# Kernel optimization log

Measured on AMD Instinct MI355X. Metric: run time of the kernel, lower is better.

The kernel has to match this reference:

```python
import jax, jax.numpy as jnp
import numpy as np

N = 50000      # nodes
E = 800000     # edges (avg degree 16)
IN_DIM = 128
HID = 64       # num_hidden
HEADS = 1
NUM_LAYERS = 3       # -> 4 SNATConv layers total
SLOPE = 0.2          # negative_slope
THR = 0.01           # threhold: edges with attention < THR are pruned after layer 0


def setup_inputs() -> dict:
    key = jax.random.key(0)
    ks = jax.random.split(key, 16)
    s = 0.05
    x = jax.random.normal(ks[0], (N, IN_DIM), jnp.float32)
    edge_src = jax.random.randint(ks[1], (E,), 0, N)
    edge_dst = jax.random.randint(ks[2], (E,), 0, N)
    W_embed = jax.random.normal(ks[3], (IN_DIM, HID), jnp.float32) * s
    n_conv = NUM_LAYERS + 1
    # all conv layers map HID*HEADS -> HEADS*HID (heads==1 so square)
    W_gat = jax.random.normal(ks[4], (n_conv, HID, HEADS * HID), jnp.float32) * s
    a_l = jax.random.normal(ks[5], (n_conv, HEADS, HID), jnp.float32) * s
    a_r = jax.random.normal(ks[6], (n_conv, HEADS, HID), jnp.float32) * s
    d_cat = (NUM_LAYERS + 1) * HID
    W0 = jax.random.normal(ks[7], (d_cat, HID), jnp.float32) * s
    b0 = jnp.zeros((HID,), jnp.float32)
    W1 = jax.random.normal(ks[8], (HID, HID), jnp.float32) * s
    b1 = jnp.zeros((HID,), jnp.float32)
    W2 = jax.random.normal(ks[9], (HID, 1), jnp.float32) * s
    b2 = jnp.zeros((1,), jnp.float32)
    return {"x": x, "edge_src": edge_src, "edge_dst": edge_dst,
            "W_embed": W_embed, "W_gat": W_gat, "a_l": a_l, "a_r": a_r,
            "W0": W0, "b0": b0, "W1": W1, "b1": b1, "W2": W2, "b2": b2}


def _edge_softmax(e, dst):
    # e: [E, H] raw scores; softmax over incoming edges of each dst node
    m = jax.ops.segment_max(e, dst, num_segments=N)       # [N, H]
    a = jnp.exp(e - m[dst])
    s = jax.ops.segment_sum(a, dst, num_segments=N)       # [N, H]
    return a / jnp.maximum(s[dst], 1e-9)


def _snat_conv(h, W, al, ar, src, dst, mask):
    # h: [N, F_in]; W: [F_in, H*HID]; al/ar: [H, HID]
    feat = (h @ W).reshape(N, HEADS, HID)                 # [N, H, HID]
    el = jnp.sum(feat * al, axis=-1)                      # [N, H]
    er = jnp.sum(feat * ar, axis=-1)
    e = jax.nn.leaky_relu(el[src] + er[dst], SLOPE)       # [E, H]
    if mask is not None:
        e = jnp.where(mask, e, -1e9)                      # prune thresholded edges
    alpha = _edge_softmax(e, dst)                         # [E, H]
    out = jax.ops.segment_sum(feat[src] * alpha[..., None], dst, num_segments=N)
    return jax.nn.elu(out), alpha                         # [N, H, HID], [E, H]


def reference(x, edge_src, edge_dst, W_embed, W_gat, a_l, a_r, W0, b0, W1, b1, W2, b2):
    src, dst = edge_src, edge_dst
    h = jnp.tanh(x @ W_embed)                             # [N, HID]
    # layer 0: computes attention and the threshold mask (index_1 / index_0)
    h0, alpha = _snat_conv(h, W_gat[0], a_l[0], a_r[0], src, dst, None)
    mask = alpha >= THR                                   # [E, H] kept-edge mask
    h = h0.reshape(N, HEADS * HID)
    H_cat = [h]
    for l in range(1, NUM_LAYERS):                        # middle layers reuse mask
        hl, _ = _snat_conv(h, W_gat[l], a_l[l], a_r[l], src, dst, mask)
        h = hl.reshape(N, HEADS * HID)
        H_cat.append(h)
    feats, _ = _snat_conv(h, W_gat[NUM_LAYERS], a_l[NUM_LAYERS], a_r[NUM_LAYERS], src, dst, mask)
    feats = feats.mean(axis=1)                            # [N, HID] mean over heads
    f = jnp.concatenate(H_cat + [feats], axis=1)          # [N, (L+1)*HID]
    out = jax.nn.relu(f @ W0 + b0)                        # activationP
    out = jax.nn.relu(out @ W1 + b1)
    out = jax.nn.relu(out @ W2 + b2)                      # final F.relu
    return out                                            # [N, 1]
```

## Files before the change

kernel.cpp:

```cpp
#include <hip/hip_runtime.h>
#include <math.h>


__global__ void k_zero(int* __restrict__ counts, int N) {
  int i = blockIdx.x * 256 + threadIdx.x;
  if (i < N) counts[i] = 0;
}

__global__ void k_hist(const int* __restrict__ dst, int* __restrict__ counts, int E) {
  int e = blockIdx.x * blockDim.x + threadIdx.x;
  if (e < E) atomicAdd(&counts[dst[e]], 1);
}

__global__ __launch_bounds__(1024) void k_bsum(const int* __restrict__ counts,
                                               int* __restrict__ bsum, int n) {
  __shared__ int wsum[16];
  int tid = threadIdx.x, lane = tid & 63, wid = tid >> 6;
  int i = blockIdx.x * 1024 + tid;
  int v = (i < n) ? counts[i] : 0;
  #pragma unroll
  for (int off = 32; off; off >>= 1) v += __shfl_xor(v, off, 64);
  if (lane == 0) wsum[wid] = v;
  __syncthreads();
  if (wid == 0) {
    int w = (lane < 16) ? wsum[lane] : 0;
    #pragma unroll
    for (int off = 8; off; off >>= 1) w += __shfl_xor(w, off, 64);
    if (lane == 0) bsum[blockIdx.x] = w;
  }
}

__global__ __launch_bounds__(64) void k_bscan(const int* __restrict__ bsum,
                                              int* __restrict__ bofs,
                                              int* __restrict__ row_ptr,
                                              int nb, int n) {
  int lane = threadIdx.x;
  int carry = 0;
  for (int base = 0; base < nb; base += 64) {
    int idx = base + lane;
    int orig = (idx < nb) ? bsum[idx] : 0;
    int inc = orig;
    #pragma unroll
    for (int off = 1; off < 64; off <<= 1) {
      int t = __shfl_up(inc, off, 64);
      if (lane >= off) inc += t;
    }
    if (idx < nb) bofs[idx] = carry + inc - orig;
    carry += __shfl(inc, 63, 64);
  }
  if (lane == 0) row_ptr[n] = carry;
}

__global__ __launch_bounds__(1024) void k_scan3(const int* __restrict__ counts,
                                                const int* __restrict__ bofs,
                                                int* __restrict__ row_ptr,
                                                int* __restrict__ cursor, int n) {
  __shared__ int wsum[16];
  int tid = threadIdx.x, lane = tid & 63, wid = tid >> 6;
  int i = blockIdx.x * 1024 + tid;
  int v = (i < n) ? counts[i] : 0;
  int inc = v;
  #pragma unroll
  for (int off = 1; off < 64; off <<= 1) {
    int t = __shfl_up(inc, off, 64);
    if (lane >= off) inc += t;
  }
  if (lane == 63) wsum[wid] = inc;
  __syncthreads();
  if (wid == 0 && lane < 16) {
    int orig = wsum[lane];
    int w = orig;
    #pragma unroll
    for (int off = 1; off < 16; off <<= 1) {
      int t = __shfl_up(w, off, 64);
      if (lane >= off) w += t;
    }
    wsum[lane] = w - orig;
  }
  __syncthreads();
  int excl = bofs[blockIdx.x] + wsum[wid] + inc - v;
  if (i < n) { row_ptr[i] = excl; cursor[i] = excl; }
}

__global__ void k_scatter(const int* __restrict__ src, const int* __restrict__ dst,
                          int* __restrict__ cursor, int* __restrict__ csr_src, int E) {
  int e = blockIdx.x * blockDim.x + threadIdx.x;
  if (e < E) {
    int pos = atomicAdd(&cursor[dst[e]], 1);
    csr_src[pos] = src[e];
  }
}

__global__ __launch_bounds__(256, 4) void k_embed_feat(
    const float* __restrict__ x, const float* __restrict__ We,
    const float* __restrict__ Wg, const float* __restrict__ al,
    const float* __restrict__ ar, float* __restrict__ feat,
    float* __restrict__ el, float* __restrict__ er, int N) {
  __shared__ float sA[64 * 129];
  __shared__ float sE[64 * 8];
  int tid = threadIdx.x, lane = tid & 63, wv = tid >> 6;
  int nb0 = blockIdx.x * 64, nl = N - 1;
  int r = tid >> 2, p = tid & 3;
  {
    const float* gp = x + (size_t)min(nb0 + r, nl) * 128;
    #pragma unroll
    for (int half = 0; half < 2; half++) {
      const float* g = gp + half * 64 + p * 16;
      float4 v0 = *(const float4*)(g + 0), v1 = *(const float4*)(g + 4);
      float4 v2 = *(const float4*)(g + 8), v3 = *(const float4*)(g + 12);
      float* dp = &sA[r * 129 + half * 64 + p * 16];
      dp[0]=v0.x; dp[1]=v0.y; dp[2]=v0.z; dp[3]=v0.w;
      dp[4]=v1.x; dp[5]=v1.y; dp[6]=v1.z; dp[7]=v1.w;
      dp[8]=v2.x; dp[9]=v2.y; dp[10]=v2.z; dp[11]=v2.w;
      dp[12]=v3.x; dp[13]=v3.y; dp[14]=v3.z; dp[15]=v3.w;
    }
  }
  __syncthreads();
  int f0 = __builtin_amdgcn_readfirstlane(wv * 16);
  float acc[16];
  #pragma unroll
  for (int f = 0; f < 16; f++) acc[f] = 0.f;
  #pragma unroll 8
  for (int k = 0; k < 128; k++) {
    float ak = sA[lane * 129 + k];
    const float* wr = We + k * 64 + f0;
    #pragma unroll
    for (int f = 0; f < 16; f++) acc[f] = fmaf(ak, wr[f], acc[f]);
  }
  __syncthreads();
  #pragma unroll
  for (int f = 0; f < 16; f++) sA[lane * 65 + f0 + f] = tanhf(acc[f]);
  __syncthreads();
  float acc2[16];
  #pragma unroll
  for (int f = 0; f < 16; f++) acc2[f] = 0.f;
  #pragma unroll 8
  for (int k = 0; k < 64; k++) {
    float ak = sA[lane * 65 + k];
    const float* wr = Wg + k * 64 + f0;
    #pragma unroll
    for (int f = 0; f < 16; f++) acc2[f] = fmaf(ak, wr[f], acc2[f]);
  }
  float rl = 0.f, rr = 0.f;
  #pragma unroll
  for (int f = 0; f < 16; f++) {
    rl = fmaf(acc2[f], al[f0 + f], rl);
    rr = fmaf(acc2[f], ar[f0 + f], rr);
  }
  sE[lane * 8 + wv] = rl;
  sE[lane * 8 + 4 + wv] = rr;
  __syncthreads();
  #pragma unroll
  for (int f = 0; f < 16; f++) sA[lane * 65 + f0 + f] = acc2[f];
  __syncthreads();
  {
    int n = nb0 + r;
    if (n < N) {
      const float* sp = &sA[r * 65 + p * 16];
      float* gp = feat + (size_t)n * 64 + p * 16;
      #pragma unroll
      for (int q = 0; q < 4; q++)
        *(float4*)(gp + q * 4) = make_float4(sp[q*4+0], sp[q*4+1], sp[q*4+2], sp[q*4+3]);
    }
  }
  if (tid < 64) {
    int n = nb0 + tid;
    if (n < N) {
      el[n] = (sE[tid*8+0] + sE[tid*8+1]) + (sE[tid*8+2] + sE[tid*8+3]);
      er[n] = (sE[tid*8+4] + sE[tid*8+5]) + (sE[tid*8+6] + sE[tid*8+7]);
    }
  }
}

__global__ __launch_bounds__(256, 4) void k_feat(const float* __restrict__ hin,
                                                 const float* __restrict__ Wg,
                                                 const float* __restrict__ al,
                                                 const float* __restrict__ ar,
                                                 float* __restrict__ feat,
                                                 float* __restrict__ el,
                                                 float* __restrict__ er, int N) {
  __shared__ float sA[64 * 65];
  __shared__ float sE[64 * 8];
  int tid = threadIdx.x, lane = tid & 63, wv = tid >> 6;
  int nb0 = blockIdx.x * 64;
  int nl = N - 1;
  int r = tid >> 2, p = tid & 3;
  {
    const float* g = hin + (size_t)min(nb0 + r, nl) * 64 + p * 16;
    float4 v0 = *(const float4*)(g + 0), v1 = *(const float4*)(g + 4);
    float4 v2 = *(const float4*)(g + 8), v3 = *(const float4*)(g + 12);
    float* dp = &sA[r * 65 + p * 16];
    dp[0]=v0.x; dp[1]=v0.y; dp[2]=v0.z; dp[3]=v0.w;
    dp[4]=v1.x; dp[5]=v1.y; dp[6]=v1.z; dp[7]=v1.w;
    dp[8]=v2.x; dp[9]=v2.y; dp[10]=v2.z; dp[11]=v2.w;
    dp[12]=v3.x; dp[13]=v3.y; dp[14]=v3.z; dp[15]=v3.w;
  }
  __syncthreads();
  int f0 = __builtin_amdgcn_readfirstlane(wv * 16);
  float acc[16];
  #pragma unroll
  for (int f = 0; f < 16; f++) acc[f] = 0.f;
  #pragma unroll 8
  for (int k = 0; k < 64; k++) {
    float ak = sA[lane * 65 + k];
    const float* wr = Wg + k * 64 + f0;
    #pragma unroll
    for (int f = 0; f < 16; f++) acc[f] = fmaf(ak, wr[f], acc[f]);
  }
  float rl = 0.f, rr = 0.f;
  #pragma unroll
  for (int f = 0; f < 16; f++) {
    rl = fmaf(acc[f], al[f0 + f], rl);
    rr = fmaf(acc[f], ar[f0 + f], rr);
  }
  __syncthreads();
  #pragma unroll
  for (int f = 0; f < 16; f++) sA[lane * 65 + f0 + f] = acc[f];
  sE[lane * 8 + wv] = rl;
  sE[lane * 8 + 4 + wv] = rr;
  __syncthreads();
  {
    int n = nb0 + r;
    if (n < N) {
      const float* sp = &sA[r * 65 + p * 16];
      float* gp = feat + (size_t)n * 64 + p * 16;
      #pragma unroll
      for (int q = 0; q < 4; q++)
        *(float4*)(gp + q * 4) = make_float4(sp[q*4+0], sp[q*4+1], sp[q*4+2], sp[q*4+3]);
    }
  }
  if (tid < 64) {
    int n = nb0 + tid;
    if (n < N) {
      el[n] = (sE[tid*8+0] + sE[tid*8+1]) + (sE[tid*8+2] + sE[tid*8+3]);
      er[n] = (sE[tid*8+4] + sE[tid*8+5]) + (sE[tid*8+6] + sE[tid*8+7]);
    }
  }
}

__global__ __launch_bounds__(256) void k_aggr(const float* __restrict__ feat,
                                              const float* __restrict__ el,
                                              const float* __restrict__ er,
                                              const int* __restrict__ row_ptr,
                                              const int* __restrict__ csr_src,
                                              unsigned char* __restrict__ mask,
                                              int write_mask, int use_mask,
                                              float* __restrict__ hout, int N) {
  __shared__ __align__(16) int   su[4][64];
  __shared__ __align__(16) float spl[4][64];
  int wv = (int)((blockIdx.x * blockDim.x + threadIdx.x) >> 6);
  int wave = threadIdx.x >> 6, lane = threadIdx.x & 63;
  if (wv >= N) return;
  int beg = row_ptr[wv], end = row_ptr[wv + 1];
  int deg = end - beg;
  float erv = er[wv];
  float acc0 = 0.f, acc1 = 0.f, acc2 = 0.f, acc3 = 0.f;
  if (deg <= 64) {
    int k = beg + lane;
    bool have = (lane < deg);
    int u = have ? csr_src[k] : 0;
    float sc = -INFINITY;
    if (have) {
      float e0 = el[u] + erv;
      sc = (e0 >= 0.f) ? e0 : 0.2f * e0;
      if (use_mask && mask[k] == 0) sc = -1e9f;
    }
    float m = sc;
    #pragma unroll
    for (int off = 32; off; off >>= 1) m = fmaxf(m, __shfl_xor(m, off, 64));
    float pl = have ? expf(sc - m) : 0.f;
    float s = pl;
    #pragma unroll
    for (int off = 32; off; off >>= 1) s += __shfl_xor(s, off, 64);
    pl *= 1.0f / fmaxf(s, 1e-9f);
    if (write_mask && have) mask[k] = (pl >= 0.01f) ? 1 : 0;
    su[wave][lane] = u;
    spl[wave][lane] = pl;
    int dq = (deg + 3) >> 2;
    #pragma unroll 2
    for (int q = 0; q < dq; q++) {
      int4   uu = *(const int4*)&su[wave][q * 4];
      float4 pp = *(const float4*)&spl[wave][q * 4];
      acc0 = fmaf(pp.x, feat[(size_t)uu.x * 64 + lane], acc0);
      acc1 = fmaf(pp.y, feat[(size_t)uu.y * 64 + lane], acc1);
      acc2 = fmaf(pp.z, feat[(size_t)uu.z * 64 + lane], acc2);
      acc3 = fmaf(pp.w, feat[(size_t)uu.w * 64 + lane], acc3);
    }
  } else {
    float m = -INFINITY, s = 0.f;
    for (int base = beg; base < end; base += 64) {
      int k = base + lane;
      float sc = -INFINITY;
      if (k < end) {
        int u = csr_src[k];
        float e0 = el[u] + erv;
        sc = (e0 >= 0.f) ? e0 : 0.2f * e0;
        if (use_mask && mask[k] == 0) sc = -1e9f;
      }
      float cm = sc;
      #pragma unroll
      for (int off = 32; off; off >>= 1) cm = fmaxf(cm, __shfl_xor(cm, off, 64));
      float nm = fmaxf(m, cm);
      float t = (k < end) ? expf(sc - nm) : 0.f;
      #pragma unroll
      for (int off = 32; off; off >>= 1) t += __shfl_xor(t, off, 64);
      s = s * expf(m - nm) + t;
      m = nm;
    }
    float inv = 1.0f / fmaxf(s, 1e-9f);
    for (int base = beg; base < end; base += 64) {
      int k = base + lane;
      int u = 0;
      float pl = 0.f;
      if (k < end) {
        u = csr_src[k];
        float e0 = el[u] + erv;
        float sc = (e0 >= 0.f) ? e0 : 0.2f * e0;
        if (use_mask && mask[k] == 0) sc = -1e9f;
        pl = expf(sc - m) * inv;
        if (write_mask) mask[k] = (pl >= 0.01f) ? 1 : 0;
      }
      su[wave][lane] = u;
      spl[wave][lane] = pl;
      int cnt = min(64, end - base);
      int dq = (cnt + 3) >> 2;
      for (int q = 0; q < dq; q++) {
        int4   uu = *(const int4*)&su[wave][q * 4];
        float4 pp = *(const float4*)&spl[wave][q * 4];
        acc0 = fmaf(pp.x, feat[(size_t)uu.x * 64 + lane], acc0);
        acc1 = fmaf(pp.y, feat[(size_t)uu.y * 64 + lane], acc1);
        acc2 = fmaf(pp.z, feat[(size_t)uu.z * 64 + lane], acc2);
        acc3 = fmaf(pp.w, feat[(size_t)uu.w * 64 + lane], acc3);
      }
    }
  }
  float acc = (acc0 + acc1) + (acc2 + acc3);
  hout[(size_t)wv * 64 + lane] = (acc > 0.f) ? acc : expm1f(acc);
}

__global__ __launch_bounds__(256, 4) void k_mlp(const float* __restrict__ o0,
                                                const float* __restrict__ o1,
                                                const float* __restrict__ o2,
                                                const float* __restrict__ o3,
                                                const float* __restrict__ W0,
                                                const float* __restrict__ b0,
                                                const float* __restrict__ W1,
                                                const float* __restrict__ b1,
                                                const float* __restrict__ W2,
                                                const float* __restrict__ b2,
                                                float* __restrict__ out, int N) {
  __shared__ float sA[64 * 65];
  __shared__ float sR[64 * 5];
  int tid = threadIdx.x, lane = tid & 63, wv = tid >> 6;
  int nb0 = blockIdx.x * 64;
  int nl = N - 1;
  int f0 = __builtin_amdgcn_readfirstlane(wv * 16);
  float acc[16];
  #pragma unroll
  for (int f = 0; f < 16; f++) acc[f] = b0[f0 + f];
  int r = tid >> 2, p = tid & 3;

  auto seg = [&](const float* __restrict__ sp, const float* __restrict__ wp) {
    __syncthreads();
    {
      const float* g = sp + (size_t)min(nb0 + r, nl) * 64 + p * 16;
      float4 v0 = *(const float4*)(g + 0), v1 = *(const float4*)(g + 4);
      float4 v2 = *(const float4*)(g + 8), v3 = *(const float4*)(g + 12);
      float* dp = &sA[r * 65 + p * 16];
      dp[0]=v0.x; dp[1]=v0.y; dp[2]=v0.z; dp[3]=v0.w;
      dp[4]=v1.x; dp[5]=v1.y; dp[6]=v1.z; dp[7]=v1.w;
      dp[8]=v2.x; dp[9]=v2.y; dp[10]=v2.z; dp[11]=v2.w;
      dp[12]=v3.x; dp[13]=v3.y; dp[14]=v3.z; dp[15]=v3.w;
    }
    __syncthreads();
    #pragma unroll 8
    for (int k = 0; k < 64; k++) {
      float ak = sA[lane * 65 + k];
      const float* wr = wp + k * 64 + f0;
      #pragma unroll
      for (int f = 0; f < 16; f++) acc[f] = fmaf(ak, wr[f], acc[f]);
    }
  };
  seg(o0, W0);
  seg(o1, W0 + 64 * 64);
  seg(o2, W0 + 128 * 64);
  seg(o3, W0 + 192 * 64);

  __syncthreads();
  #pragma unroll
  for (int f = 0; f < 16; f++)
    sA[lane * 65 + f0 + f] = (acc[f] > 0.f) ? acc[f] : 0.f;
  __syncthreads();
  float a1[16];
  #pragma unroll
  for (int f = 0; f < 16; f++) a1[f] = b1[f0 + f];
  #pragma unroll 8
  for (int k = 0; k < 64; k++) {
    float ak = sA[lane * 65 + k];
    const float* wr = W1 + k * 64 + f0;
    #pragma unroll
    for (int f = 0; f < 16; f++) a1[f] = fmaf(ak, wr[f], a1[f]);
  }
  float rp = 0.f;
  #pragma unroll
  for (int f = 0; f < 16; f++) {
    float t = (a1[f] > 0.f) ? a1[f] : 0.f;
    rp = fmaf(t, W2[f0 + f], rp);
  }
  sR[lane * 5 + wv] = rp;
  __syncthreads();
  if (tid < 64) {
    int n = nb0 + tid;
    if (n < N) {
      float o = (sR[tid*5+0] + sR[tid*5+1]) + (sR[tid*5+2] + sR[tid*5+3]) + b2[0];
      out[n] = (o > 0.f) ? o : 0.f;
    }
  }
}

extern "C" void kernel_launch(void* const* d_in, const int* in_sizes, int n_in,
                              void* d_out, int out_size, void* d_ws, size_t ws_size,
                              hipStream_t stream) {
  const float* x       = (const float*)d_in[0];
  const int*   esrc    = (const int*)d_in[1];
  const int*   edst    = (const int*)d_in[2];
  const float* W_embed = (const float*)d_in[3];
  const float* W_gat   = (const float*)d_in[4];
  const float* a_l     = (const float*)d_in[5];
  const float* a_r     = (const float*)d_in[6];
  const float* W0      = (const float*)d_in[7];
  const float* b0      = (const float*)d_in[8];
  const float* W1      = (const float*)d_in[9];
  const float* b1      = (const float*)d_in[10];
  const float* W2      = (const float*)d_in[11];
  const float* b2      = (const float*)d_in[12];
  float* out = (float*)d_out;
  const int N = in_sizes[0] / 128;
  const int E = in_sizes[1];

  char* p = (char*)d_ws;
  auto alloc = [&](size_t bytes) -> char* {
    char* r = p;
    p += (bytes + 255) & ~(size_t)255;
    return r;
  };
  float* out0 = (float*)alloc((size_t)N * 64 * 4);
  float* out1 = (float*)alloc((size_t)N * 64 * 4);
  float* out2 = (float*)alloc((size_t)N * 64 * 4);
  float* out3 = (float*)alloc((size_t)N * 64 * 4);
  float* feat = (float*)alloc((size_t)N * 64 * 4);
  float* el   = (float*)alloc((size_t)N * 4);
  float* er   = (float*)alloc((size_t)N * 4);
  int* counts  = (int*)alloc((size_t)N * 4);
  int* row_ptr = (int*)alloc((size_t)(N + 1) * 4);
  int* cursor  = (int*)alloc((size_t)N * 4);
  int* csr_src = (int*)alloc((size_t)E * 4);
  unsigned char* mask = (unsigned char*)alloc((size_t)E);
  int nb = (N + 1023) / 1024;
  int* bsum = (int*)alloc((size_t)nb * 4);
  int* bofs = (int*)alloc((size_t)nb * 4);

  k_zero<<<(N + 255) / 256, 256, 0, stream>>>(counts, N);
  k_hist<<<(E + 255) / 256, 256, 0, stream>>>(edst, counts, E);
  k_bsum<<<nb, 1024, 0, stream>>>(counts, bsum, N);
  k_bscan<<<1, 64, 0, stream>>>(bsum, bofs, row_ptr, nb, N);
  k_scan3<<<nb, 1024, 0, stream>>>(counts, bofs, row_ptr, cursor, N);
  k_scatter<<<(E + 255) / 256, 256, 0, stream>>>(esrc, edst, cursor, csr_src, E);

  int dgb = (N + 63) / 64;

  k_embed_feat<<<dgb, 256, 0, stream>>>(x, W_embed, W_gat,
                                        a_l, a_r, feat, el, er, N);
  float* outs[4] = {out0, out1, out2, out3};
  k_aggr<<<(N + 3) / 4, 256, 0, stream>>>(feat, el, er, row_ptr, csr_src, mask,
                                          1, 0, out0, N);

  for (int l = 1; l < 4; l++) {
    k_feat<<<dgb, 256, 0, stream>>>(outs[l - 1], W_gat + (size_t)l * 4096,
                                    a_l + (size_t)l * 64, a_r + (size_t)l * 64,
                                    feat, el, er, N);
    k_aggr<<<(N + 3) / 4, 256, 0, stream>>>(feat, el, er, row_ptr, csr_src, mask,
                                            0, 1, outs[l], N);
  }

  k_mlp<<<dgb, 256, 0, stream>>>(out0, out1, out2, out3, W0, b0,
                                 W1, b1, W2, b2, out, N);
}
```

Baseline: 453.2 us.

## Register-tile dense GEMM kernels 4x8 per thread with weights staged in LDS

Rewrites the embed, feature and MLP dense-transform kernels to use 4-node by 8-feature register tiles per thread. Weight matrices are staged into shared memory, and activations are read directly from global memory with vector loads. Each block now covers 128 nodes instead of 64, and the attention dot-product partials are reduced with shuffles. The goal is to cut repeated global weight loads and raise FMA reuse per load, at the cost of more registers and larger LDS use that may lower occupancy.

```diff
diff --git a/kernel.cpp b/kernel.cpp
--- a/kernel.cpp
+++ b/kernel.cpp
@@ -91,84 +91,160 @@
   }
 }
 
+#define LOAD8(A, P)                                                  \
+  {                                                                  \
+    float4 v0_ = *(const float4*)(P);                                \
+    float4 v1_ = *(const float4*)((P) + 4);                          \
+    A[0] = v0_.x; A[1] = v0_.y; A[2] = v0_.z; A[3] = v0_.w;          \
+    A[4] = v1_.x; A[5] = v1_.y; A[6] = v1_.z; A[7] = v1_.w;          \
+  }
+
+#define STAGE_W(DST, SRC, TID)                                       \
+  {                                                                  \
+    const float4* s4_ = (const float4*)(SRC);                        \
+    float4* d4_ = (float4*)(DST);                                    \
+    _Pragma("unroll")                                                \
+    for (int i_ = 0; i_ < 4; i_++)                                   \
+      d4_[(TID) + 256 * i_] = s4_[(TID) + 256 * i_];                 \
+  }
+
 __global__ __launch_bounds__(256, 4) void k_embed_feat(
     const float* __restrict__ x, const float* __restrict__ We,
     const float* __restrict__ Wg, const float* __restrict__ al,
     const float* __restrict__ ar, float* __restrict__ feat,
     float* __restrict__ el, float* __restrict__ er, int N) {
-  __shared__ float sA[64 * 129];
-  __shared__ float sE[64 * 8];
+  __shared__ float sW[64 * 64];
+  __shared__ float sH[128 * 65];
+  __shared__ float sEl[256], sEr[256];
   int tid = threadIdx.x, lane = tid & 63, wv = tid >> 6;
-  int nb0 = blockIdx.x * 64, nl = N - 1;
-  int r = tid >> 2, p = tid & 3;
-  {
-    const float* gp = x + (size_t)min(nb0 + r, nl) * 128;
-    #pragma unroll
-    for (int half = 0; half < 2; half++) {
-      const float* g = gp + half * 64 + p * 16;
-      float4 v0 = *(const float4*)(g + 0), v1 = *(const float4*)(g + 4);
-      float4 v2 = *(const float4*)(g + 8), v3 = *(const float4*)(g + 12);
-      float* dp = &sA[r * 129 + half * 64 + p * 16];
-      dp[0]=v0.x; dp[1]=v0.y; dp[2]=v0.z; dp[3]=v0.w;
-      dp[4]=v1.x; dp[5]=v1.y; dp[6]=v1.z; dp[7]=v1.w;
-      dp[8]=v2.x; dp[9]=v2.y; dp[10]=v2.z; dp[11]=v2.w;
-      dp[12]=v3.x; dp[13]=v3.y; dp[14]=v3.z; dp[15]=v3.w;
-    }
-  }
-  __syncthreads();
-  int f0 = __builtin_amdgcn_readfirstlane(wv * 16);
-  float acc[16];
-  #pragma unroll
-  for (int f = 0; f < 16; f++) acc[f] = 0.f;
-  #pragma unroll 8
-  for (int k = 0; k < 128; k++) {
-    float ak = sA[lane * 129 + k];
-    const float* wr = We + k * 64 + f0;
-    #pragma unroll
-    for (int f = 0; f < 16; f++) acc[f] = fmaf(ak, wr[f], acc[f]);
-  }
-  __syncthreads();
-  #pragma unroll
-  for (int f = 0; f < 16; f++) sA[lane * 65 + f0 + f] = tanhf(acc[f]);
-  __syncthreads();
-  float acc2[16];
-  #pragma unroll
-  for (int f = 0; f < 16; f++) acc2[f] = 0.f;
-  #pragma unroll 8
+  int nb0 = blockIdx.x * 128, nl_max = N - 1;
+  int tile = wv >> 1, fh = wv & 1;
+  int g = lane & 15, q = lane >> 4;
+  int f0 = fh * 32 + q * 8;
+  int n0 = nb0 + tile * 64 + g * 4;
+  const float* xp0 = x + (size_t)min(n0 + 0, nl_max) * 128;
+  const float* xp1 = x + (size_t)min(n0 + 1, nl_max) * 128;
+  const float* xp2 = x + (size_t)min(n0 + 2, nl_max) * 128;
+  const float* xp3 = x + (size_t)min(n0 + 3, nl_max) * 128;
+
+  float acc[4][8];
+  #pragma unroll
+  for (int i = 0; i < 4; i++)
+    #pragma unroll
+    for (int j = 0; j < 8; j++) acc[i][j] = 0.f;
+
+  STAGE_W(sW, We, tid);
+  __syncthreads();
+  #pragma unroll 2
+  for (int kc = 0; kc < 64; kc += 8) {
+    float a0[8], a1[8], a2[8], a3[8];
+    LOAD8(a0, xp0 + kc); LOAD8(a1, xp1 + kc);
+    LOAD8(a2, xp2 + kc); LOAD8(a3, xp3 + kc);
+    #pragma unroll
+    for (int kk = 0; kk < 8; kk++) {
+      float w[8];
+      *(float4*)&w[0] = *(const float4*)&sW[(kc + kk) * 64 + f0];
+      *(float4*)&w[4] = *(const float4*)&sW[(kc + kk) * 64 + f0 + 4];
+      #pragma unroll
+      for (int j = 0; j < 8; j++) {
+        acc[0][j] = fmaf(a0[kk], w[j], acc[0][j]);
+        acc[1][j] = fmaf(a1[kk], w[j], acc[1][j]);
+        acc[2][j] = fmaf(a2[kk], w[j], acc[2][j]);
+        acc[3][j] = fmaf(a3[kk], w[j], acc[3][j]);
+      }
+    }
+  }
+  __syncthreads();
+  STAGE_W(sW, We + 4096, tid);
+  __syncthreads();
+  #pragma unroll 2
+  for (int kc = 64; kc < 128; kc += 8) {
+    float a0[8], a1[8], a2[8], a3[8];
+    LOAD8(a0, xp0 + kc); LOAD8(a1, xp1 + kc);
+    LOAD8(a2, xp2 + kc); LOAD8(a3, xp3 + kc);
+    #pragma unroll
+    for (int kk = 0; kk < 8; kk++) {
+      float w[8];
+      *(float4*)&w[0] = *(const float4*)&sW[(kc - 64 + kk) * 64 + f0];
+      *(float4*)&w[4] = *(const float4*)&sW[(kc - 64 + kk) * 64 + f0 + 4];
+      #pragma unroll
+      for (int j = 0; j < 8; j++) {
+        acc[0][j] = fmaf(a0[kk], w[j], acc[0][j]);
+        acc[1][j] = fmaf(a1[kk], w[j], acc[1][j]);
+        acc[2][j] = fmaf(a2[kk], w[j], acc[2][j]);
+        acc[3][j] = fmaf(a3[kk], w[j], acc[3][j]);
+      }
+    }
+  }
+  __syncthreads();
+  STAGE_W(sW, Wg, tid);
+  #pragma unroll
+  for (int i = 0; i < 4; i++) {
+    int hb = (tile * 64 + g * 4 + i) * 65 + f0;
+    #pragma unroll
+    for (int j = 0; j < 8; j++) sH[hb + j] = tanhf(acc[i][j]);
+  }
+  __syncthreads();
+
+  float acc2[4][8];
+  #pragma unroll
+  for (int i = 0; i < 4; i++)
+    #pragma unroll
+    for (int j = 0; j < 8; j++) acc2[i][j] = 0.f;
+  int hb0 = (tile * 64 + g * 4 + 0) * 65;
+  int hb1 = hb0 + 65, hb2 = hb0 + 130, hb3 = hb0 + 195;
+  #pragma unroll 4
   for (int k = 0; k < 64; k++) {
-    float ak = sA[lane * 65 + k];
-    const float* wr = Wg + k * 64 + f0;
-    #pragma unroll
-    for (int f = 0; f < 16; f++) acc2[f] = fmaf(ak, wr[f], acc2[f]);
-  }
-  float rl = 0.f, rr = 0.f;
-  #pragma unroll
-  for (int f = 0; f < 16; f++) {
-    rl = fmaf(acc2[f], al[f0 + f], rl);
-    rr = fmaf(acc2[f], ar[f0 + f], rr);
-  }
-  sE[lane * 8 + wv] = rl;
-  sE[lane * 8 + 4 + wv] = rr;
-  __syncthreads();
-  #pragma unroll
-  for (int f = 0; f < 16; f++) sA[lane * 65 + f0 + f] = acc2[f];
-  __syncthreads();
-  {
-    int n = nb0 + r;
+    float w[8];
+    *(float4*)&w[0] = *(const float4*)&sW[k * 64 + f0];
+    *(float4*)&w[4] = *(const float4*)&sW[k * 64 + f0 + 4];
+    float h0 = sH[hb0 + k], h1 = sH[hb1 + k], h2 = sH[hb2 + k], h3 = sH[hb3 + k];
+    #pragma unroll
+    for (int j = 0; j < 8; j++) {
+      acc2[0][j] = fmaf(h0, w[j], acc2[0][j]);
+      acc2[1][j] = fmaf(h1, w[j], acc2[1][j]);
+      acc2[2][j] = fmaf(h2, w[j], acc2[2][j]);
+      acc2[3][j] = fmaf(h3, w[j], acc2[3][j]);
+    }
+  }
+  float alv[8], arv[8];
+  *(float4*)&alv[0] = *(const float4*)(al + f0);
+  *(float4*)&alv[4] = *(const float4*)(al + f0 + 4);
+  *(float4*)&arv[0] = *(const float4*)(ar + f0);
+  *(float4*)&arv[4] = *(const float4*)(ar + f0 + 4);
+  #pragma unroll
+  for (int i = 0; i < 4; i++) {
+    float pl = 0.f, pr = 0.f;
+    #pragma unroll
+    for (int j = 0; j < 8; j++) {
+      pl = fmaf(acc2[i][j], alv[j], pl);
+      pr = fmaf(acc2[i][j], arv[j], pr);
+    }
+    pl += __shfl_xor(pl, 16, 64); pl += __shfl_xor(pl, 32, 64);
+    pr += __shfl_xor(pr, 16, 64); pr += __shfl_xor(pr, 32, 64);
+    if (lane < 16) {
+      int nl = tile * 64 + g * 4 + i;
+      sEl[nl * 2 + fh] = pl;
+      sEr[nl * 2 + fh] = pr;
+    }
+  }
+  #pragma unroll
+  for (int i = 0; i < 4; i++) {
+    int n = n0 + i;
     if (n < N) {
-      const float* sp = &sA[r * 65 + p * 16];
-      float* gp = feat + (size_t)n * 64 + p * 16;
-      #pragma unroll
-      for (int q = 0; q < 4; q++)
-        *(float4*)(gp + q * 4) = make_float4(sp[q*4+0], sp[q*4+1], sp[q*4+2], sp[q*4+3]);
-    }
-  }
-  if (tid < 64) {
+      *(float4*)(feat + (size_t)n * 64 + f0) =
+          make_float4(acc2[i][0], acc2[i][1], acc2[i][2], acc2[i][3]);
+      *(float4*)(feat + (size_t)n * 64 + f0 + 4) =
+          make_float4(acc2[i][4], acc2[i][5], acc2[i][6], acc2[i][7]);
+    }
+  }
+  __syncthreads();
+  if (tid < 128) {
     int n = nb0 + tid;
-    if (n < N) {
-      el[n] = (sE[tid*8+0] + sE[tid*8+1]) + (sE[tid*8+2] + sE[tid*8+3]);
-      er[n] = (sE[tid*8+4] + sE[tid*8+5]) + (sE[tid*8+6] + sE[tid*8+7]);
-    }
+    if (n < N) el[n] = sEl[tid * 2] + sEl[tid * 2 + 1];
+  } else {
+    int t = tid - 128, n = nb0 + t;
+    if (n < N) er[n] = sEr[t * 2] + sEr[t * 2 + 1];
   }
 }
 
@@ -179,62 +255,84 @@
                                                  float* __restrict__ feat,
                                                  float* __restrict__ el,
                                                  float* __restrict__ er, int N) {
-  __shared__ float sA[64 * 65];
-  __shared__ float sE[64 * 8];
+  __shared__ float sW[64 * 64];
+  __shared__ float sEl[256], sEr[256];
   int tid = threadIdx.x, lane = tid & 63, wv = tid >> 6;
-  int nb0 = blockIdx.x * 64;
-  int nl = N - 1;
-  int r = tid >> 2, p = tid & 3;
-  {
-    const float* g = hin + (size_t)min(nb0 + r, nl) * 64 + p * 16;
-    float4 v0 = *(const float4*)(g + 0), v1 = *(const float4*)(g + 4);
-    float4 v2 = *(const float4*)(g + 8), v3 = *(const float4*)(g + 12);
-    float* dp = &sA[r * 65 + p * 16];
-    dp[0]=v0.x; dp[1]=v0.y; dp[2]=v0.z; dp[3]=v0.w;
-    dp[4]=v1.x; dp[5]=v1.y; dp[6]=v1.z; dp[7]=v1.w;
-    dp[8]=v2.x; dp[9]=v2.y; dp[10]=v2.z; dp[11]=v2.w;
-    dp[12]=v3.x; dp[13]=v3.y; dp[14]=v3.z; dp[15]=v3.w;
-  }
-  __syncthreads();
-  int f0 = __builtin_amdgcn_readfirstlane(wv * 16);
-  float acc[16];
-  #pragma unroll
-  for (int f = 0; f < 16; f++) acc[f] = 0.f;
-  #pragma unroll 8
-  for (int k = 0; k < 64; k++) {
-    float ak = sA[lane * 65 + k];
-    const float* wr = Wg + k * 64 + f0;
-    #pragma unroll
-    for (int f = 0; f < 16; f++) acc[f] = fmaf(ak, wr[f], acc[f]);
-  }
-  float rl = 0.f, rr = 0.f;
-  #pragma unroll
-  for (int f = 0; f < 16; f++) {
-    rl = fmaf(acc[f], al[f0 + f], rl);
-    rr = fmaf(acc[f], ar[f0 + f], rr);
-  }
-  __syncthreads();
-  #pragma unroll
-  for (int f = 0; f < 16; f++) sA[lane * 65 + f0 + f] = acc[f];
-  sE[lane * 8 + wv] = rl;
-  sE[lane * 8 + 4 + wv] = rr;
-  __syncthreads();
-  {
-    int n = nb0 + r;
+  int nb0 = blockIdx.x * 128, nl_max = N - 1;
+  int tile = wv >> 1, fh = wv & 1;
+  int g = lane & 15, q = lane >> 4;
+  int f0 = fh * 32 + q * 8;
+  int n0 = nb0 + tile * 64 + g * 4;
+  const float* bp0 = hin + (size_t)min(n0 + 0, nl_max) * 64;
+  const float* bp1 = hin + (size_t)min(n0 + 1, nl_max) * 64;
+  const float* bp2 = hin + (size_t)min(n0 + 2, nl_max) * 64;
+  const float* bp3 = hin + (size_t)min(n0 + 3, nl_max) * 64;
+
+  STAGE_W(sW, Wg, tid);
+  __syncthreads();
+
+  float acc[4][8];
+  #pragma unroll
+  for (int i = 0; i < 4; i++)
+    #pragma unroll
+    for (int j = 0; j < 8; j++) acc[i][j] = 0.f;
+  #pragma unroll 2
+  for (int kc = 0; kc < 64; kc += 8) {
+    float a0[8], a1[8], a2[8], a3[8];
+    LOAD8(a0, bp0 + kc); LOAD8(a1, bp1 + kc);
+    LOAD8(a2, bp2 + kc); LOAD8(a3, bp3 + kc);
+    #pragma unroll
+    for (int kk = 0; kk < 8; kk++) {
+      float w[8];
+      *(float4*)&w[0] = *(const float4*)&sW[(kc + kk) * 64 + f0];
+      *(float4*)&w[4] = *(const float4*)&sW[(kc + kk) * 64 + f0 + 4];
+      #pragma unroll
+      for (int j = 0; j < 8; j++) {
+        acc[0][j] = fmaf(a0[kk], w[j], acc[0][j]);
+        acc[1][j] = fmaf(a1[kk], w[j], acc[1][j]);
+        acc[2][j] = fmaf(a2[kk], w[j], acc[2][j]);
+        acc[3][j] = fmaf(a3[kk], w[j], acc[3][j]);
+      }
+    }
+  }
+  float alv[8], arv[8];
+  *(float4*)&alv[0] = *(const float4*)(al + f0);
+  *(float4*)&alv[4] = *(const float4*)(al + f0 + 4);
+  *(float4*)&arv[0] = *(const float4*)(ar + f0);
+  *(float4*)&arv[4] = *(const float4*)(ar + f0 + 4);
+  #pragma unroll
+  for (int i = 0; i < 4; i++) {
+    float pl = 0.f, pr = 0.f;
+    #pragma unroll
+    for (int j = 0; j < 8; j++) {
+      pl = fmaf(acc[i][j], alv[j], pl);
+      pr = fmaf(acc[i][j], arv[j], pr);
+    }
+    pl += __shfl_xor(pl, 16, 64); pl += __shfl_xor(pl, 32, 64);
+    pr += __shfl_xor(pr, 16, 64); pr += __shfl_xor(pr, 32, 64);
+    if (lane < 16) {
+      int nl = tile * 64 + g * 4 + i;
+      sEl[nl * 2 + fh] = pl;
+      sEr[nl * 2 + fh] = pr;
+    }
+  }
+  #pragma unroll
+  for (int i = 0; i < 4; i++) {
+    int n = n0 + i;
     if (n < N) {
-      const float* sp = &sA[r * 65 + p * 16];
-      float* gp = feat + (size_t)n * 64 + p * 16;
-      #pragma unroll
-      for (int q = 0; q < 4; q++)
-        *(float4*)(gp + q * 4) = make_float4(sp[q*4+0], sp[q*4+1], sp[q*4+2], sp[q*4+3]);
-    }
-  }
-  if (tid < 64) {
+      *(float4*)(feat + (size_t)n * 64 + f0) =
+          make_float4(acc[i][0], acc[i][1], acc[i][2], acc[i][3]);
+      *(float4*)(feat + (size_t)n * 64 + f0 + 4) =
+          make_float4(acc[i][4], acc[i][5], acc[i][6], acc[i][7]);
+    }
+  }
+  __syncthreads();
+  if (tid < 128) {
     int n = nb0 + tid;
-    if (n < N) {
-      el[n] = (sE[tid*8+0] + sE[tid*8+1]) + (sE[tid*8+2] + sE[tid*8+3]);
-      er[n] = (sE[tid*8+4] + sE[tid*8+5]) + (sE[tid*8+6] + sE[tid*8+7]);
-    }
+    if (n < N) el[n] = sEl[tid * 2] + sEl[tid * 2 + 1];
+  } else {
+    int t = tid - 128, n = nb0 + t;
+    if (n < N) er[n] = sEr[t * 2] + sEr[t * 2 + 1];
   }
 }
 
@@ -278,9 +376,9 @@
     spl[wave][lane] = pl;
     int dq = (deg + 3) >> 2;
     #pragma unroll 2
-    for (int q = 0; q < dq; q++) {
-      int4   uu = *(const int4*)&su[wave][q * 4];
-      float4 pp = *(const float4*)&spl[wave][q * 4];
+    for (int qq = 0; qq < dq; qq++) {
+      int4   uu = *(const int4*)&su[wave][qq * 4];
+      float4 pp = *(const float4*)&spl[wave][qq * 4];
       acc0 = fmaf(pp.x, feat[(size_t)uu.x * 64 + lane], acc0);
       acc1 = fmaf(pp.y, feat[(size_t)uu.y * 64 + lane], acc1);
       acc2 = fmaf(pp.z, feat[(size_t)uu.z * 64 + lane], acc2);
@@ -324,9 +422,9 @@
       spl[wave][lane] = pl;
       int cnt = min(64, end - base);
       int dq = (cnt + 3) >> 2;
-      for (int q = 0; q < dq; q++) {
-        int4   uu = *(const int4*)&su[wave][q * 4];
-        float4 pp = *(const float4*)&spl[wave][q * 4];
+      for (int qq = 0; qq < dq; qq++) {
+        int4   uu = *(const int4*)&su[wave][qq * 4];
+        float4 pp = *(const float4*)&spl[wave][qq * 4];
         acc0 = fmaf(pp.x, feat[(size_t)uu.x * 64 + lane], acc0);
         acc1 = fmaf(pp.y, feat[(size_t)uu.y * 64 + lane], acc1);
         acc2 = fmaf(pp.z, feat[(size_t)uu.z * 64 + lane], acc2);
@@ -349,36 +447,53 @@
                                                 const float* __restrict__ W2,
                                                 const float* __restrict__ b2,
                                                 float* __restrict__ out, int N) {
-  __shared__ float sA[64 * 65];
-  __shared__ float sR[64 * 5];
+  __shared__ float sW[64 * 64];
+  __shared__ float sH[128 * 65];
+  __shared__ float sR[256];
   int tid = threadIdx.x, lane = tid & 63, wv = tid >> 6;
-  int nb0 = blockIdx.x * 64;
-  int nl = N - 1;
-  int f0 = __builtin_amdgcn_readfirstlane(wv * 16);
-  float acc[16];
-  #pragma unroll
-  for (int f = 0; f < 16; f++) acc[f] = b0[f0 + f];
-  int r = tid >> 2, p = tid & 3;
+  int nb0 = blockIdx.x * 128, nl_max = N - 1;
+  int tile = wv >> 1, fh = wv & 1;
+  int g = lane & 15, q = lane >> 4;
+  int f0 = fh * 32 + q * 8;
+  int n0 = nb0 + tile * 64 + g * 4;
+
+  float acc[4][8];
+  {
+    float b0v[8];
+    *(float4*)&b0v[0] = *(const float4*)(b0 + f0);
+    *(float4*)&b0v[4] = *(const float4*)(b0 + f0 + 4);
+    #pragma unroll
+    for (int i = 0; i < 4; i++)
+      #pragma unroll
+      for (int j = 0; j < 8; j++) acc[i][j] = b0v[j];
+  }
 
   auto seg = [&](const float* __restrict__ sp, const float* __restrict__ wp) {
     __syncthreads();
-    {
-      const float* g = sp + (size_t)min(nb0 + r, nl) * 64 + p * 16;
-      float4 v0 = *(const float4*)(g + 0), v1 = *(const float4*)(g + 4);
-      float4 v2 = *(const float4*)(g + 8), v3 = *(const float4*)(g + 12);
-      float* dp = &sA[r * 65 + p * 16];
-      dp[0]=v0.x; dp[1]=v0.y; dp[2]=v0.z; dp[3]=v0.w;
-      dp[4]=v1.x; dp[5]=v1.y; dp[6]=v1.z; dp[7]=v1.w;
-      dp[8]=v2.x; dp[9]=v2.y; dp[10]=v2.z; dp[11]=v2.w;
-      dp[12]=v3.x; dp[13]=v3.y; dp[14]=v3.z; dp[15]=v3.w;
-    }
+    STAGE_W(sW, wp, tid);
     __syncthreads();
-    #pragma unroll 8
-    for (int k = 0; k < 64; k++) {
-      float ak = sA[lane * 65 + k];
-      const float* wr = wp + k * 64 + f0;
-      #pragma unroll
-      for (int f = 0; f < 16; f++) acc[f] = fmaf(ak, wr[f], acc[f]);
+    const float* bp0 = sp + (size_t)min(n0 + 0, nl_max) * 64;
+    const float* bp1 = sp + (size_t)min(n0 + 1, nl_max) * 64;
+    const float* bp2 = sp + (size_t)min(n0 + 2, nl_max) * 64;
+    const float* bp3 = sp + (size_t)min(n0 + 3, nl_max) * 64;
+    #pragma unroll 2
+    for (int kc = 0; kc < 64; kc += 8) {
+      float a0[8], a1[8], a2[8], a3[8];
+      LOAD8(a0, bp0 + kc); LOAD8(a1, bp1 + kc);
+      LOAD8(a2, bp2 + kc); LOAD8(a3, bp3 + kc);
+      #pragma unroll
+      for (int kk = 0; kk < 8; kk++) {
+        float w[8];
+        *(float4*)&w[0] = *(const float4*)&sW[(kc + kk) * 64 + f0];
+        *(float4*)&w[4] = *(const float4*)&sW[(kc + kk) * 64 + f0 + 4];
+        #pragma unroll
+        for (int j = 0; j < 8; j++) {
+          acc[0][j] = fmaf(a0[kk], w[j], acc[0][j]);
+          acc[1][j] = fmaf(a1[kk], w[j], acc[1][j]);
+          acc[2][j] = fmaf(a2[kk], w[j], acc[2][j]);
+          acc[3][j] = fmaf(a3[kk], w[j], acc[3][j]);
+        }
+      }
     }
   };
   seg(o0, W0);
@@ -387,32 +502,61 @@
   seg(o3, W0 + 192 * 64);
 
   __syncthreads();
-  #pragma unroll
-  for (int f = 0; f < 16; f++)
-    sA[lane * 65 + f0 + f] = (acc[f] > 0.f) ? acc[f] : 0.f;
-  __syncthreads();
-  float a1[16];
-  #pragma unroll
-  for (int f = 0; f < 16; f++) a1[f] = b1[f0 + f];
-  #pragma unroll 8
+  STAGE_W(sW, W1, tid);
+  #pragma unroll
+  for (int i = 0; i < 4; i++) {
+    int hb = (tile * 64 + g * 4 + i) * 65 + f0;
+    #pragma unroll
+    for (int j = 0; j < 8; j++)
+      sH[hb + j] = (acc[i][j] > 0.f) ? acc[i][j] : 0.f;
+  }
+  __syncthreads();
+
+  float a1v[4][8];
+  {
+    float b1v[8];
+    *(float4*)&b1v[0] = *(const float4*)(b1 + f0);
+    *(float4*)&b1v[4] = *(const float4*)(b1 + f0 + 4);
+    #pragma unroll
+    for (int i = 0; i < 4; i++)
+      #pragma unroll
+      for (int j = 0; j < 8; j++) a1v[i][j] = b1v[j];
+  }
+  int hb0 = (tile * 64 + g * 4 + 0) * 65;
+  int hb1 = hb0 + 65, hb2 = hb0 + 130, hb3 = hb0 + 195;
+  #pragma unroll 4
   for (int k = 0; k < 64; k++) {
-    float ak = sA[lane * 65 + k];
-    const float* wr = W1 + k * 64 + f0;
-    #pragma unroll
-    for (int f = 0; f < 16; f++) a1[f] = fmaf(ak, wr[f], a1[f]);
-  }
-  float rp = 0.f;
-  #pragma unroll
-  for (int f = 0; f < 16; f++) {
-    float t = (a1[f] > 0.f) ? a1[f] : 0.f;
-    rp = fmaf(t, W2[f0 + f], rp);
-  }
-  sR[lane * 5 + wv] = rp;
-  __syncthreads();
-  if (tid < 64) {
+    float w[8];
+    *(float4*)&w[0] = *(const float4*)&sW[k * 64 + f0];
+    *(float4*)&w[4] = *(const float4*)&sW[k * 64 + f0 + 4];
+    float h0 = sH[hb0 + k], h1 = sH[hb1 + k], h2 = sH[hb2 + k], h3 = sH[hb3 + k];
+    #pragma unroll
+    for (int j = 0; j < 8; j++) {
+      a1v[0][j] = fmaf(h0, w[j], a1v[0][j]);
+      a1v[1][j] = fmaf(h1, w[j], a1v[1][j]);
+      a1v[2][j] = fmaf(h2, w[j], a1v[2][j]);
+      a1v[3][j] = fmaf(h3, w[j], a1v[3][j]);
+    }
+  }
+  float w2v[8];
+  *(float4*)&w2v[0] = *(const float4*)(W2 + f0);
+  *(float4*)&w2v[4] = *(const float4*)(W2 + f0 + 4);
+  #pragma unroll
+  for (int i = 0; i < 4; i++) {
+    float rp = 0.f;
+    #pragma unroll
+    for (int j = 0; j < 8; j++) {
+      float t = (a1v[i][j] > 0.f) ? a1v[i][j] : 0.f;
+      rp = fmaf(t, w2v[j], rp);
+    }
+    rp += __shfl_xor(rp, 16, 64); rp += __shfl_xor(rp, 32, 64);
+    if (lane < 16) sR[(tile * 64 + g * 4 + i) * 2 + fh] = rp;
+  }
+  __syncthreads();
+  if (tid < 128) {
     int n = nb0 + tid;
     if (n < N) {
-      float o = (sR[tid*5+0] + sR[tid*5+1]) + (sR[tid*5+2] + sR[tid*5+3]) + b2[0];
+      float o = sR[tid * 2] + sR[tid * 2 + 1] + b2[0];
       out[n] = (o > 0.f) ? o : 0.f;
     }
   }
@@ -467,7 +611,7 @@
   k_scan3<<<nb, 1024, 0, stream>>>(counts, bofs, row_ptr, cursor, N);
   k_scatter<<<(E + 255) / 256, 256, 0, stream>>>(esrc, edst, cursor, csr_src, E);
 
-  int dgb = (N + 63) / 64;
+  int dgb = (N + 127) / 128;
 
   k_embed_feat<<<dgb, 256, 0, stream>>>(x, W_embed, W_gat,
                                         a_l, a_r, feat, el, er, N);
```

After: 509.8 us. 1.12x slower.
